# Kernel tuning notes

Hardware: AMD Instinct MI355X
Metric: run time of the kernel (lower is better)

The kernel has to match this reference:

```python
import jax, jax.numpy as jnp
import numpy as np

N_NODES = 50000
N_EDGES = 600000
H_DIM = 128
N_RELS = 8
N_BASES = 4


def setup_inputs() -> dict:
    key = jax.random.key(0)
    ks = jax.random.split(key, 12)
    feats = jax.random.normal(ks[0], (N_NODES, H_DIM), dtype=jnp.float32)
    src = jax.random.randint(ks[1], (N_EDGES,), 0, N_NODES, dtype=jnp.int64)
    dst = jax.random.randint(ks[2], (N_EDGES,), 0, N_NODES, dtype=jnp.int64)
    etype = jax.random.randint(ks[3], (N_EDGES,), 0, N_RELS, dtype=jnp.int64)
    norm = jax.random.uniform(ks[4], (N_EDGES, 1), dtype=jnp.float32)
    s = 1.0 / np.sqrt(H_DIM)
    # layer 0 params (basis decomposition: W_r = sum_b comp[r,b] * basis[b])
    basis0 = jax.random.normal(ks[5], (N_BASES, H_DIM, H_DIM), dtype=jnp.float32) * s
    comp0 = jax.random.normal(ks[6], (N_RELS, N_BASES), dtype=jnp.float32)
    bias0 = jnp.zeros((H_DIM,), dtype=jnp.float32)
    # layer 1 params
    basis1 = jax.random.normal(ks[7], (N_BASES, H_DIM, H_DIM), dtype=jnp.float32) * s
    comp1 = jax.random.normal(ks[8], (N_RELS, N_BASES), dtype=jnp.float32)
    bias1 = jnp.zeros((H_DIM,), dtype=jnp.float32)
    return {"feats": feats, "src": src, "dst": dst, "etype": etype, "norm": norm,
            "basis0": basis0, "comp0": comp0, "bias0": bias0,
            "basis1": basis1, "comp1": comp1, "bias1": bias1}


def _rel_graph_conv(h, src, dst, etype, norm, basis, comp, bias):
    # basis-decomposed relation weights: [R, d_in, d_out]
    W = jnp.einsum('rb,bdo->rdo', comp, basis)
    # transform all nodes under every relation: [R, N, d_out]
    Hr = jnp.einsum('nd,rdo->rno', h, W)
    # gather per-edge message by (relation, source node), apply edge norm
    msg = Hr[etype, src] * norm  # [E, d_out]
    # scatter-sum into destination nodes
    agg = jax.ops.segment_sum(msg, dst, num_segments=h.shape[0])
    return jax.nn.relu(agg + bias)


def reference(feats, src, dst, etype, norm, basis0, comp0, bias0, basis1, comp1, bias1):
    h = _rel_graph_conv(feats, src, dst, etype, norm, basis0, comp0, bias0)
    h = _rel_graph_conv(h, src, dst, etype, norm, basis1, comp1, bias1)
    return h
```

## Files before the change

### kernel.cpp

```cpp
#include <hip/hip_runtime.h>

#define H    128
#define NB   4

typedef __attribute__((ext_vector_type(8))) short short8;
typedef __attribute__((ext_vector_type(4))) float f32x4;

static __device__ __forceinline__ unsigned short f2bf(float f) {
    unsigned u = __float_as_uint(f);
    unsigned r = (u + 0x7fffu + ((u >> 16) & 1u)) >> 16;
    return (unsigned short)r;
}
static __device__ __forceinline__ float bfe(short s) {
    return __uint_as_float(((unsigned)(unsigned short)s) << 16);
}

__global__ __launch_bounds__(256) void hist_rank(const int* __restrict__ dst,
                                                 int* __restrict__ counts,
                                                 int* __restrict__ rank, int E) {
    int e = blockIdx.x * 256 + threadIdx.x;
    if (e < E) rank[e] = atomicAdd(&counts[dst[e]], 1);
}

__global__ __launch_bounds__(1024) void scan_blocks(const int* __restrict__ counts,
                                                    int* __restrict__ partial,
                                                    int* __restrict__ blocksums, int n) {
    __shared__ int buf[1024];
    int tid = threadIdx.x;
    int i = blockIdx.x * 1024 + tid;
    buf[tid] = (i < n) ? counts[i] : 0;
    __syncthreads();
#pragma unroll
    for (int off = 1; off < 1024; off <<= 1) {
        int t = (tid >= off) ? buf[tid - off] : 0;
        __syncthreads();
        buf[tid] += t;
        __syncthreads();
    }
    if (i < n) partial[i] = buf[tid];
    if (tid == 1023) blocksums[blockIdx.x] = buf[1023];
}

__global__ __launch_bounds__(64) void scan_carry(int* __restrict__ blocksums, int nb) {
    int tid = threadIdx.x;
    int v = (tid < nb) ? blocksums[tid] : 0;
#pragma unroll
    for (int off = 1; off < 64; off <<= 1) {
        int t = __shfl_up(v, off);
        if (tid >= off) v += t;
    }
    if (tid < nb) blocksums[tid] = v;
}

__global__ __launch_bounds__(256) void scan_add(const int* __restrict__ partial,
                                                const int* __restrict__ blocksums,
                                                int* __restrict__ offs, int n) {
    int i = blockIdx.x * 256 + threadIdx.x;
    if (i >= n) return;
    int b = i >> 10;
    int carry = (b > 0) ? blocksums[b - 1] : 0;
    offs[i + 1] = partial[i] + carry;
    if (i == 0) offs[0] = 0;
}

__global__ __launch_bounds__(256) void scatter_edges(
        const int* __restrict__ src, const int* __restrict__ dst,
        const int* __restrict__ etype, const float* __restrict__ norm,
        const int* __restrict__ offs, const int* __restrict__ rank,
        uint2* __restrict__ er, int E) {
    int e = blockIdx.x * 256 + threadIdx.x;
    if (e >= E) return;
    int pos = offs[dst[e]] + rank[e];
    uint2 r;
    r.x = (unsigned)src[e] | ((unsigned)etype[e] << 17);
    r.y = __float_as_uint(norm[e]);
    er[pos] = r;
}

__global__ __launch_bounds__(256) void convert_bf16(const float* __restrict__ in,
                                                    unsigned short* __restrict__ out, int n4) {
    int i = blockIdx.x * 256 + threadIdx.x;
    if (i >= n4) return;
    float4 v = ((const float4*)in)[i];
    ushort4 o;
    o.x = f2bf(v.x); o.y = f2bf(v.y); o.z = f2bf(v.z); o.w = f2bf(v.w);
    ((ushort4*)out)[i] = o;
}

__global__ __launch_bounds__(128) void make_wb(
        const float* __restrict__ basis0, const float* __restrict__ basis1,
        unsigned short* __restrict__ Wb) {
    int b = blockIdx.x;
    int d = blockIdx.y;
    int l = blockIdx.z;
    int o = threadIdx.x;
    const float* basis = l ? basis1 : basis0;
    float s = basis[((size_t)b * H + d) * H + o];
    Wb[((size_t)l * H + o) * (NB * H) + b * H + d] = f2bf(s);
}

#define EACC(WA, WB, WC, WD, HV) {                                      \
    _Pragma("unroll")                                                   \
    for (int c = 0; c < 8; ++c) {                                       \
        float f = bfe(HV[c]);                                           \
        a0[c] = fmaf(WA, f, a0[c]); a1[c] = fmaf(WB, f, a1[c]);         \
        a2[c] = fmaf(WC, f, a2[c]); a3[c] = fmaf(WD, f, a3[c]);         \
    } }

__global__ __launch_bounds__(256, 8) void agg_nodes(
        const unsigned short* __restrict__ hin,
        const int* __restrict__ offs,
        const uint2* __restrict__ er,
        const float* __restrict__ comp,
        unsigned short* __restrict__ agg,
        int M) {
    __shared__ float cmp[32];
    const int tid = threadIdx.x;
    if (tid < 32) cmp[tid] = comp[tid];
    __syncthreads();

    const int nl  = tid >> 4;
    const int ch  = tid & 15;
    const int v   = blockIdx.x * 16 + nl;
    if (v >= M) return;

    float a0[8], a1[8], a2[8], a3[8];
#pragma unroll
    for (int c = 0; c < 8; ++c) { a0[c] = 0.f; a1[c] = 0.f; a2[c] = 0.f; a3[c] = 0.f; }

    const int beg = offs[v], end = offs[v + 1];
    int e = beg;
    for (; e + 2 <= end; e += 2) {
        uint2 r0 = er[e];
        uint2 r1 = er[e + 1];
        short8 h0 = *(const short8*)(hin + (size_t)(r0.x & 0x1FFFF) * H + ch * 8);
        short8 h1 = *(const short8*)(hin + (size_t)(r1.x & 0x1FFFF) * H + ch * 8);
        {
            const float* c0 = cmp + (r0.x >> 17) * 4;
            float w = __uint_as_float(r0.y);
            float wa = w * c0[0], wb = w * c0[1], wc = w * c0[2], wd = w * c0[3];
            EACC(wa, wb, wc, wd, h0)
        }
        {
            const float* c1 = cmp + (r1.x >> 17) * 4;
            float w = __uint_as_float(r1.y);
            float wa = w * c1[0], wb = w * c1[1], wc = w * c1[2], wd = w * c1[3];
            EACC(wa, wb, wc, wd, h1)
        }
    }
    if (e < end) {
        uint2 r0 = er[e];
        short8 h0 = *(const short8*)(hin + (size_t)(r0.x & 0x1FFFF) * H + ch * 8);
        const float* c0 = cmp + (r0.x >> 17) * 4;
        float w = __uint_as_float(r0.y);
        float wa = w * c0[0], wb = w * c0[1], wc = w * c0[2], wd = w * c0[3];
        EACC(wa, wb, wc, wd, h0)
    }

    unsigned short* orow = agg + (size_t)v * (NB * H) + ch * 8;
    uint4 pk;
#define PACK(A) pk.x = (unsigned)f2bf(A[0]) | ((unsigned)f2bf(A[1]) << 16); \
                pk.y = (unsigned)f2bf(A[2]) | ((unsigned)f2bf(A[3]) << 16); \
                pk.z = (unsigned)f2bf(A[4]) | ((unsigned)f2bf(A[5]) << 16); \
                pk.w = (unsigned)f2bf(A[6]) | ((unsigned)f2bf(A[7]) << 16);
    PACK(a0) *(uint4*)(orow + 0 * H) = pk;
    PACK(a1) *(uint4*)(orow + 1 * H) = pk;
    PACK(a2) *(uint4*)(orow + 2 * H) = pk;
    PACK(a3) *(uint4*)(orow + 3 * H) = pk;
#undef PACK
}

__global__ __launch_bounds__(512) void gemm_out(
        const unsigned short* __restrict__ agg,
        const unsigned short* __restrict__ Wb,
        const float* __restrict__ bias,
        void* __restrict__ outp, int M, int write_bf16) {
    __shared__ char lds[32 * 1024];
    const int tid  = threadIdx.x;
    const int v0   = blockIdx.x * 32;

#pragma unroll
    for (int i = 0; i < 4; ++i) {
        int id  = tid + i * 512;
        int row = id >> 6;
        int c16 = id & 63;
        int gr  = min(v0 + row, M - 1);
        uint4 vld = *(const uint4*)((const char*)agg + (size_t)gr * 1024 + c16 * 16);
        *(uint4*)(lds + row * 1024 + ((c16 * 16) ^ ((row & 7) << 4))) = vld;
    }
    __syncthreads();

    const int wid  = tid >> 6;
    const int lane = tid & 63;
    const int n0 = wid * 16;
    const int lr = lane & 15;
    const int lg = lane >> 4;
    const char* bbase = (const char*)Wb + (size_t)(n0 + lr) * (NB * H) * 2;
    const int swz = (lr & 7) << 4;

    f32x4 acc0 = (f32x4){0.f, 0.f, 0.f, 0.f};
    f32x4 acc1 = (f32x4){0.f, 0.f, 0.f, 0.f};
#pragma unroll
    for (int ks = 0; ks < 16; ++ks) {
        const int kb = ks * 64 + lg * 16;
        short8 b   = *(const short8*)(bbase + kb);
        short8 av0 = *(const short8*)(lds + (lr)      * 1024 + (kb ^ swz));
        short8 av1 = *(const short8*)(lds + (16 + lr) * 1024 + (kb ^ swz));
        acc0 = __builtin_amdgcn_mfma_f32_16x16x32_bf16(av0, b, acc0, 0, 0, 0);
        acc1 = __builtin_amdgcn_mfma_f32_16x16x32_bf16(av1, b, acc1, 0, 0, 0);
    }

    const float bcol = bias[n0 + lr];
#pragma unroll
    for (int m = 0; m < 2; ++m) {
        const f32x4 a = m ? acc1 : acc0;
#pragma unroll
        for (int j = 0; j < 4; ++j) {
            const int rl   = m * 16 + lg * 4 + j;
            const int grow = v0 + rl;
            if (grow < M) {
                float val = fmaxf(a[j] + bcol, 0.f);
                if (write_bf16)
                    ((unsigned short*)outp)[(size_t)grow * H + n0 + lr] = f2bf(val);
                else
                    ((float*)outp)[(size_t)grow * H + n0 + lr] = val;
            }
        }
    }
}

extern "C" void kernel_launch(void* const* d_in, const int* in_sizes, int n_in,
                              void* d_out, int out_size, void* d_ws, size_t ws_size,
                              hipStream_t stream) {
    const float* feats  = (const float*)d_in[0];
    const int*   src    = (const int*)  d_in[1];
    const int*   dst    = (const int*)  d_in[2];
    const int*   etype  = (const int*)  d_in[3];
    const float* norm   = (const float*)d_in[4];
    const float* basis0 = (const float*)d_in[5];
    const float* comp0  = (const float*)d_in[6];
    const float* bias0  = (const float*)d_in[7];
    const float* basis1 = (const float*)d_in[8];
    const float* comp1  = (const float*)d_in[9];
    const float* bias1  = (const float*)d_in[10];
    float* out = (float*)d_out;

    const int M = in_sizes[0] / H;
    const int E = in_sizes[1];

    char* ws = (char*)d_ws;
    size_t cur = 0;
    auto take = [&](size_t bytes) { void* p = ws + cur; cur += (bytes + 255) & ~(size_t)255; return p; };
    unsigned short* hbf  = (unsigned short*)take((size_t)M * H * 2);
    unsigned short* h1bf = (unsigned short*)take((size_t)M * H * 2);
    unsigned short* agg  = (unsigned short*)take((size_t)M * NB * H * 2);
    unsigned short* Wb   = (unsigned short*)take((size_t)2 * H * NB * H * 2);
    int*   counts  = (int*)take((size_t)M * 4);
    int*   offs    = (int*)take((size_t)(M + 1) * 4);
    int*   partial = (int*)take((size_t)M * 4);
    int*   bsums   = (int*)take((size_t)64 * 4);
    int*   rank    = (int*)take((size_t)E * 4);
    uint2* er      = (uint2*)take((size_t)E * 8);

    dim3 blk(256);
    int eb  = (E + 255) / 256;
    int n4  = M * H / 4;
    int cb  = (n4 + 255) / 256;
    int mb  = (M + 255) / 256;
    int nsb = (M + 1023) / 1024;
    int ab  = (M + 15) / 16;
    int gb  = (M + 31) / 32;

    hipMemsetAsync(counts, 0, (size_t)M * 4, stream);
    hist_rank    <<<eb, blk, 0, stream>>>(dst, counts, rank, E);
    scan_blocks  <<<nsb, 1024, 0, stream>>>(counts, partial, bsums, M);
    scan_carry   <<<1, 64, 0, stream>>>(bsums, nsb);
    scan_add     <<<mb, blk, 0, stream>>>(partial, bsums, offs, M);
    scatter_edges<<<eb, blk, 0, stream>>>(src, dst, etype, norm, offs, rank, er, E);
    convert_bf16 <<<cb, blk, 0, stream>>>(feats, hbf, n4);
    make_wb      <<<dim3(NB, H, 2), 128, 0, stream>>>(basis0, basis1, Wb);

    agg_nodes<<<ab, blk, 0, stream>>>(hbf, offs, er, comp0, agg, M);
    gemm_out <<<gb, 512, 0, stream>>>(agg, Wb, bias0, h1bf, M, 1);
    agg_nodes<<<ab, blk, 0, stream>>>(h1bf, offs, er, comp1, agg, M);
    gemm_out <<<gb, 512, 0, stream>>>(agg, Wb + (size_t)H * NB * H, bias1, out, M, 0);
}
```

Before: 221.3 us.

## Fuse edge aggregation and basis GEMM into one kernel via shared memory

Merges the per-node aggregation kernel and the output GEMM kernel. The aggregated basis projections now go straight into a swizzled shared-memory tile instead of a global bf16 buffer, which removes the global write and re-read of the M x 512 agg buffer and one launch per layer. The edge loop is also unrolled from 2 to 4 edges to raise memory-level parallelism. The cost is larger 512-thread blocks, where the GEMM phase must wait for the slowest node's gather in its tile, and higher register pressure under launch_bounds(512,4).

Measured after the change: 194.6 us. 12.1% less time.

```diff
diff --git a/kernel.cpp b/kernel.cpp
--- a/kernel.cpp
+++ b/kernel.cpp
@@ -2,6 +2,7 @@
 
 #define H    128
 #define NB   4
+#define DT   32
 
 typedef __attribute__((ext_vector_type(8))) short short8;
 typedef __attribute__((ext_vector_type(4))) float f32x4;
@@ -99,94 +100,75 @@
     Wb[((size_t)l * H + o) * (NB * H) + b * H + d] = f2bf(s);
 }
 
-#define EACC(WA, WB, WC, WD, HV) {                                      \
+#define EACC(R, HV) {                                                   \
+    const float* cp = cmp + ((R.x >> 17) & 7) * 4;                      \
+    float w = __uint_as_float(R.y);                                     \
+    float wa = w * cp[0], wb = w * cp[1];                               \
+    float wc = w * cp[2], wd = w * cp[3];                               \
     _Pragma("unroll")                                                   \
     for (int c = 0; c < 8; ++c) {                                       \
         float f = bfe(HV[c]);                                           \
-        a0[c] = fmaf(WA, f, a0[c]); a1[c] = fmaf(WB, f, a1[c]);         \
-        a2[c] = fmaf(WC, f, a2[c]); a3[c] = fmaf(WD, f, a3[c]);         \
+        a0[c] = fmaf(wa, f, a0[c]); a1[c] = fmaf(wb, f, a1[c]);         \
+        a2[c] = fmaf(wc, f, a2[c]); a3[c] = fmaf(wd, f, a3[c]);         \
     } }
 
-__global__ __launch_bounds__(256, 8) void agg_nodes(
+__global__ __launch_bounds__(512, 4) void fused_layer(
         const unsigned short* __restrict__ hin,
         const int* __restrict__ offs,
         const uint2* __restrict__ er,
         const float* __restrict__ comp,
-        unsigned short* __restrict__ agg,
-        int M) {
+        const unsigned short* __restrict__ Wb,
+        const float* __restrict__ bias,
+        void* __restrict__ outp, int M, int write_bf16) {
+    __shared__ char lds[DT * 1024];
     __shared__ float cmp[32];
-    const int tid = threadIdx.x;
+    const int tid  = threadIdx.x;
     if (tid < 32) cmp[tid] = comp[tid];
     __syncthreads();
 
-    const int nl  = tid >> 4;
-    const int ch  = tid & 15;
-    const int v   = blockIdx.x * 16 + nl;
-    if (v >= M) return;
+    const int nl   = tid >> 4;
+    const int ch   = tid & 15;
+    const int v0   = blockIdx.x * DT;
+    const int v    = v0 + nl;
 
     float a0[8], a1[8], a2[8], a3[8];
 #pragma unroll
     for (int c = 0; c < 8; ++c) { a0[c] = 0.f; a1[c] = 0.f; a2[c] = 0.f; a3[c] = 0.f; }
 
-    const int beg = offs[v], end = offs[v + 1];
-    int e = beg;
-    for (; e + 2 <= end; e += 2) {
-        uint2 r0 = er[e];
-        uint2 r1 = er[e + 1];
-        short8 h0 = *(const short8*)(hin + (size_t)(r0.x & 0x1FFFF) * H + ch * 8);
-        short8 h1 = *(const short8*)(hin + (size_t)(r1.x & 0x1FFFF) * H + ch * 8);
-        {
-            const float* c0 = cmp + (r0.x >> 17) * 4;
-            float w = __uint_as_float(r0.y);
-            float wa = w * c0[0], wb = w * c0[1], wc = w * c0[2], wd = w * c0[3];
-            EACC(wa, wb, wc, wd, h0)
+    if (v < M) {
+        const int beg = offs[v], end = offs[v + 1];
+        int e = beg;
+        for (; e + 4 <= end; e += 4) {
+            uint2 r0 = er[e];
+            uint2 r1 = er[e + 1];
+            uint2 r2 = er[e + 2];
+            uint2 r3 = er[e + 3];
+            short8 h0 = *(const short8*)(hin + (size_t)(r0.x & 0x1FFFF) * H + ch * 8);
+            short8 h1 = *(const short8*)(hin + (size_t)(r1.x & 0x1FFFF) * H + ch * 8);
+            short8 h2 = *(const short8*)(hin + (size_t)(r2.x & 0x1FFFF) * H + ch * 8);
+            short8 h3 = *(const short8*)(hin + (size_t)(r3.x & 0x1FFFF) * H + ch * 8);
+            EACC(r0, h0) EACC(r1, h1) EACC(r2, h2) EACC(r3, h3)
         }
-        {
-            const float* c1 = cmp + (r1.x >> 17) * 4;
-            float w = __uint_as_float(r1.y);
-            float wa = w * c1[0], wb = w * c1[1], wc = w * c1[2], wd = w * c1[3];
-            EACC(wa, wb, wc, wd, h1)
+        for (; e < end; ++e) {
+            uint2 r0 = er[e];
+            short8 h0 = *(const short8*)(hin + (size_t)(r0.x & 0x1FFFF) * H + ch * 8);
+            EACC(r0, h0)
         }
     }
-    if (e < end) {
-        uint2 r0 = er[e];
-        short8 h0 = *(const short8*)(hin + (size_t)(r0.x & 0x1FFFF) * H + ch * 8);
-        const float* c0 = cmp + (r0.x >> 17) * 4;
-        float w = __uint_as_float(r0.y);
-        float wa = w * c0[0], wb = w * c0[1], wc = w * c0[2], wd = w * c0[3];
-        EACC(wa, wb, wc, wd, h0)
-    }
-
-    unsigned short* orow = agg + (size_t)v * (NB * H) + ch * 8;
-    uint4 pk;
+
+    {
+        char* row = lds + nl * 1024;
+        const int swz = (nl & 7) << 4;
+        uint4 pk;
 #define PACK(A) pk.x = (unsigned)f2bf(A[0]) | ((unsigned)f2bf(A[1]) << 16); \
                 pk.y = (unsigned)f2bf(A[2]) | ((unsigned)f2bf(A[3]) << 16); \
                 pk.z = (unsigned)f2bf(A[4]) | ((unsigned)f2bf(A[5]) << 16); \
                 pk.w = (unsigned)f2bf(A[6]) | ((unsigned)f2bf(A[7]) << 16);
-    PACK(a0) *(uint4*)(orow + 0 * H) = pk;
-    PACK(a1) *(uint4*)(orow + 1 * H) = pk;
-    PACK(a2) *(uint4*)(orow + 2 * H) = pk;
-    PACK(a3) *(uint4*)(orow + 3 * H) = pk;
+        PACK(a0) *(uint4*)(row + ((0 * 256 + ch * 16) ^ swz)) = pk;
+        PACK(a1) *(uint4*)(row + ((1 * 256 + ch * 16) ^ swz)) = pk;
+        PACK(a2) *(uint4*)(row + ((2 * 256 + ch * 16) ^ swz)) = pk;
+        PACK(a3) *(uint4*)(row + ((3 * 256 + ch * 16) ^ swz)) = pk;
 #undef PACK
-}
-
-__global__ __launch_bounds__(512) void gemm_out(
-        const unsigned short* __restrict__ agg,
-        const unsigned short* __restrict__ Wb,
-        const float* __restrict__ bias,
-        void* __restrict__ outp, int M, int write_bf16) {
-    __shared__ char lds[32 * 1024];
-    const int tid  = threadIdx.x;
-    const int v0   = blockIdx.x * 32;
-
-#pragma unroll
-    for (int i = 0; i < 4; ++i) {
-        int id  = tid + i * 512;
-        int row = id >> 6;
-        int c16 = id & 63;
-        int gr  = min(v0 + row, M - 1);
-        uint4 vld = *(const uint4*)((const char*)agg + (size_t)gr * 1024 + c16 * 16);
-        *(uint4*)(lds + row * 1024 + ((c16 * 16) ^ ((row & 7) << 4))) = vld;
     }
     __syncthreads();
 
@@ -253,7 +235,6 @@
     auto take = [&](size_t bytes) { void* p = ws + cur; cur += (bytes + 255) & ~(size_t)255; return p; };
     unsigned short* hbf  = (unsigned short*)take((size_t)M * H * 2);
     unsigned short* h1bf = (unsigned short*)take((size_t)M * H * 2);
-    unsigned short* agg  = (unsigned short*)take((size_t)M * NB * H * 2);
     unsigned short* Wb   = (unsigned short*)take((size_t)2 * H * NB * H * 2);
     int*   counts  = (int*)take((size_t)M * 4);
     int*   offs    = (int*)take((size_t)(M + 1) * 4);
@@ -268,8 +249,7 @@
     int cb  = (n4 + 255) / 256;
     int mb  = (M + 255) / 256;
     int nsb = (M + 1023) / 1024;
-    int ab  = (M + 15) / 16;
-    int gb  = (M + 31) / 32;
+    int fb  = (M + DT - 1) / DT;
 
     hipMemsetAsync(counts, 0, (size_t)M * 4, stream);
     hist_rank    <<<eb, blk, 0, stream>>>(dst, counts, rank, E);
@@ -280,8 +260,7 @@
     convert_bf16 <<<cb, blk, 0, stream>>>(feats, hbf, n4);
     make_wb      <<<dim3(NB, H, 2), 128, 0, stream>>>(basis0, basis1, Wb);
 
-    agg_nodes<<<ab, blk, 0, stream>>>(hbf, offs, er, comp0, agg, M);
-    gemm_out <<<gb, 512, 0, stream>>>(agg, Wb, bias0, h1bf, M, 1);
-    agg_nodes<<<ab, blk, 0, stream>>>(h1bf, offs, er, comp1, agg, M);
-    gemm_out <<<gb, 512, 0, stream>>>(agg, Wb + (size_t)H * NB * H, bias1, out, M, 0);
-}
+    fused_layer<<<fb, 512, 0, stream>>>(hbf, offs, er, comp0, Wb, bias0, h1bf, M, 1);
+    fused_layer<<<fb, 512, 0, stream>>>(h1bf, offs, er, comp1,
+                                        Wb + (size_t)H * NB * H, bias1, out, M, 0);
+}
```
